# Kernel optimization log

Measured on AMD Instinct MI355X. Metric: run time of the kernel, lower is better.

The kernel has to match this reference:

```python
import jax, jax.numpy as jnp
import numpy as np

RADIUS = 0.4
K = 32
EPS = 1e-5


def ball_query(xyz, new_xyz, radius, k):
    """xyz: (B,N,3), new_xyz: (B,M,3) -> idx (B,M,k) int32.
    Replicates CUDA ball_query: first k points within radius (in index order),
    padded with the first found index."""
    N = xyz.shape[1]
    # squared distances (B,M,N)
    d2 = jnp.sum((new_xyz[:, :, None, :] - xyz[:, None, :, :]) ** 2, axis=-1)
    within = d2 < radius * radius
    order = jnp.arange(N, dtype=jnp.int32)
    key = jnp.where(within, order[None, None, :], N)
    idx_sorted = jnp.argsort(key, axis=-1)[..., :k].astype(jnp.int32)  # (B,M,k)
    cnt = within.sum(axis=-1)  # (B,M)
    first = idx_sorted[..., :1]
    slot = jnp.arange(k)[None, None, :]
    return jnp.where(slot < cnt[..., None], idx_sorted, first)


def gather_bmk(x_bnc, idx):
    """x_bnc: (B,N,C), idx: (B,M,K) -> (B,M,K,C)"""
    return jnp.take_along_axis(x_bnc[:, None, :, :], idx[..., None], axis=2)


def conv_bn_relu(x, w, b, gamma, beta):
    """x: (B,Cin,M,K); w: (Cout,Cin). 1x1 Conv2d + BatchNorm2d (train stats) + ReLU."""
    x = jnp.einsum('bcmk,oc->bomk', x, w) + b[None, :, None, None]
    mu = x.mean(axis=(0, 2, 3), keepdims=True)
    var = x.var(axis=(0, 2, 3), keepdims=True)
    x = gamma[None, :, None, None] * (x - mu) * jax.lax.rsqrt(var + EPS) + beta[None, :, None, None]
    return jax.nn.relu(x)


def setup_inputs() -> dict:
    key = jax.random.key(0)
    ks = jax.random.split(key, 16)
    B, N, C, M = 4, 16384, 128, 1024
    mlp = [131, 128, 128, 256]
    inp = {
        'points_xyz': jax.random.normal(ks[0], (B, N, 3), dtype=jnp.float32),
        'features': jax.random.normal(ks[1], (B, C, N), dtype=jnp.float32),
        'indices': jax.random.randint(ks[2], (B, M), 0, N, dtype=jnp.int32),
    }
    for i in range(3):
        cin, cout = mlp[i], mlp[i + 1]
        inp[f'w{i+1}'] = jax.random.normal(ks[3 + 4 * i], (cout, cin), dtype=jnp.float32) / np.sqrt(cin)
        inp[f'b{i+1}'] = jnp.zeros((cout,), dtype=jnp.float32)
        inp[f'g{i+1}'] = jnp.ones((cout,), dtype=jnp.float32)
        inp[f'beta{i+1}'] = jnp.zeros((cout,), dtype=jnp.float32)
    return inp


def reference(points_xyz, features, indices,
              w1, b1, g1, beta1, w2, b2, g2, beta2, w3, b3, g3, beta3):
    # sample centers: new_xyz (B,M,3)
    new_xyz = jnp.take_along_axis(points_xyz, indices[..., None], axis=1)
    # ball query + group
    idx = ball_query(points_xyz, new_xyz, RADIUS, K)            # (B,M,K)
    grouped_xyz = gather_bmk(points_xyz, idx) - new_xyz[:, :, None, :]  # (B,M,K,3)
    grouped_feat = gather_bmk(features.transpose(0, 2, 1), idx)         # (B,M,K,C)
    x = jnp.concatenate([grouped_xyz, grouped_feat], axis=-1)           # (B,M,K,3+C)
    x = x.transpose(0, 3, 1, 2)                                         # (B,3+C,M,K)
    # shared MLP (1x1 Conv2d + BN + ReLU)
    x = conv_bn_relu(x, w1, b1, g1, beta1)
    x = conv_bn_relu(x, w2, b2, g2, beta2)
    x = conv_bn_relu(x, w3, b3, g3, beta3)
    # max pool over K -> (B, Cout, M)
    new_features = x.max(axis=-1)
    return new_xyz, new_features
```

## Files before the change

kernel.cpp:

```cpp
#include <hip/hip_runtime.h>

#define B_ 4
#define N_ 16384
#define C_ 128
#define M_ 1024
#define K_ 32
#define NTOT (B_*M_*K_)
#define RAD2 0.16f
#define EPS_ 1e-5f

typedef unsigned short ushort_t;
typedef __bf16 bf16x8 __attribute__((ext_vector_type(8)));
typedef float f32x4 __attribute__((ext_vector_type(4)));

__device__ __forceinline__ float b2f(ushort_t u){
  unsigned int x = ((unsigned int)u) << 16;
  return __builtin_bit_cast(float, x);
}
__device__ __forceinline__ ushort_t f2b(float f){
  unsigned int u = __builtin_bit_cast(unsigned int, f);
  unsigned int r = (u + 0x7FFFu + ((u >> 16) & 1u)) >> 16;
  return (ushort_t)r;
}

__global__ __launch_bounds__(256) void ball_query_k(
    const float* __restrict__ xyz, const int* __restrict__ indices,
    float* __restrict__ new_xyz, int* __restrict__ idx)
{
  int t = threadIdx.x;
  int wv = t >> 6, lane = t & 63;
  int g = blockIdx.x*4 + wv;
  int b = g >> 10;
  const float* pb = xyz + (size_t)b*N_*3;
  const float4* pb4 = (const float4*)pb;
  int qi = indices[g];
  float qx = pb[qi*3+0], qy = pb[qi*3+1], qz = pb[qi*3+2];
  if (lane < 3) new_xyz[g*3 + lane] = pb[qi*3 + lane];

  int cnt = 0, firstIdx = 0;
  int* op = idx + g*K_;

  float4 buf0[6], buf1[6];
  #pragma unroll
  for (int i = 0; i < 6; i++) buf0[i] = pb4[lane*6 + i];

  auto process = [&](const float4* buf, int chunk){
    const float* f = (const float*)buf;
    unsigned int local_mask = 0;
    #pragma unroll
    for (int j = 0; j < 8; j++){
      float dx = f[j*3+0]-qx, dy = f[j*3+1]-qy, dz = f[j*3+2]-qz;
      if (dx*dx + dy*dy + dz*dz < RAD2) local_mask |= (1u << j);
    }
    if (__ballot(local_mask != 0) == 0ull) return;
    int base = chunk*512;
    int lcnt = __popc(local_mask);
    int incl = lcnt;
    #pragma unroll
    for (int d = 1; d < 64; d <<= 1){
      int tt = __shfl_up(incl, d);
      if (lane >= d) incl += tt;
    }
    int excl = incl - lcnt;
    int total = __shfl(incl, 63);
    if (cnt == 0){
      int lf = local_mask ? (lane*8 + __builtin_ctz(local_mask)) : 0x7fffffff;
      #pragma unroll
      for (int d = 1; d < 64; d <<= 1) lf = min(lf, __shfl_xor(lf, d));
      firstIdx = base + lf;
    }
    int sl = cnt + excl;
    unsigned int m = local_mask;
    while (m && sl < K_){
      int j = __builtin_ctz(m); m &= m - 1u;
      op[sl++] = base + lane*8 + j;
    }
    cnt += total;
  };

  for (int chunk = 0; chunk < 32; chunk += 2){
    if (chunk + 1 < 32){
      #pragma unroll
      for (int i = 0; i < 6; i++) buf1[i] = pb4[(chunk+1)*384 + lane*6 + i];
    }
    process(buf0, chunk);
    if (cnt >= K_) break;
    if (chunk + 2 < 32){
      #pragma unroll
      for (int i = 0; i < 6; i++) buf0[i] = pb4[(chunk+2)*384 + lane*6 + i];
    }
    process(buf1, chunk + 1);
    if (cnt >= K_) break;
  }
  if (cnt < K_){
    for (int s = cnt + lane; s < K_; s += 64) op[s] = firstIdx;
  }
}

__global__ __launch_bounds__(256) void transpose_feat_k(
    const float* __restrict__ feat, ushort_t* __restrict__ ftr_t)
{
  __shared__ float T[32][133];
  int bi = blockIdx.x;
  int b = bi >> 9, ntile = bi & 511;
  int n0 = ntile * 32;
  int t = threadIdx.x;
  int nl = t & 31;
  #pragma unroll
  for (int ci = 0; ci < 16; ci++){
    int c = ci*8 + (t >> 5);
    T[nl][c] = feat[((size_t)b*C_ + c)*N_ + n0 + nl];
  }
  __syncthreads();
  #pragma unroll
  for (int ii = 0; ii < 2; ii++){
    int v = ii*256 + t;
    int n2 = v >> 4, seg = v & 15;
    union { ushort_t u[8]; uint4 q; } pk;
    #pragma unroll
    for (int j = 0; j < 8; j++) pk.u[j] = f2b(T[n2][seg*8 + j]);
    *(uint4*)(ftr_t + ((size_t)b*N_ + n0 + n2)*C_ + seg*8) = pk.q;
  }
}

__global__ __launch_bounds__(256) void prep_w_k(
    const float* __restrict__ w1, const float* __restrict__ w2, const float* __restrict__ w3,
    ushort_t* __restrict__ W1b, ushort_t* __restrict__ W2b, ushort_t* __restrict__ W3b)
{
  const int T1 = 128*160, T2 = 128*128, T3 = 256*128;
  for (int e = blockIdx.x*256 + threadIdx.x; e < T1+T2+T3; e += gridDim.x*256){
    if (e < T1){
      int o = e / 160, c = e % 160;
      float v = 0.f;
      if (c < 128) v = w1[o*131 + 3 + c];
      else if (c < 131) v = w1[o*131 + (c - 128)];
      W1b[e] = f2b(v);
    } else if (e < T1+T2){
      int e2 = e - T1;
      W2b[e2] = f2b(w2[e2]);
    } else {
      int e3 = e - T1 - T2;
      W3b[e3] = f2b(w3[e3]);
    }
  }
}

__global__ __launch_bounds__(256, 2) void conv1_k(
    const float* __restrict__ xyz, const ushort_t* __restrict__ ftr_t,
    const int* __restrict__ idx, const float* __restrict__ new_xyz,
    const ushort_t* __restrict__ W1b, const float* __restrict__ b1,
    ushort_t* __restrict__ Y1, float* __restrict__ sumO, float* __restrict__ sqO)
{
  __shared__ alignas(16) ushort_t Xs[32*168];
  __shared__ alignas(16) float Ys[32*68];
  int t = threadIdx.x;
  int wv = t >> 6, lane = t & 63, quad = lane >> 4, l15 = lane & 15;
  int row = t >> 3, chunk = t & 7;
  int col0 = (blockIdx.x & 1) * 64;
  int blk = blockIdx.x >> 1;

  if (t < 128){
    int rr = t >> 2, cc = t & 3;
    *(uint4*)(Xs + rr*168 + 128 + cc*8) = make_uint4(0,0,0,0);
  }
  bf16x8 wf[5];
  #pragma unroll
  for (int kt = 0; kt < 5; kt++)
    wf[kt] = *(const bf16x8*)(W1b + (col0 + wv*16 + l15)*160 + kt*32 + quad*8);
  float bs_r = b1[col0 + wv*16 + l15];
  float s = 0.f, s2 = 0.f;

  const int GPB = 8;
  int g0 = blk * GPB;
  int b = g0 >> 10;
  int ia[GPB], ibv[GPB];
  #pragma unroll
  for (int i = 0; i < GPB; i++){
    ia[i]  = idx[(g0+i)*K_ + row];
    ibv[i] = idx[(g0+i)*K_ + (t & 31)];
  }
  for (int i = 0; i < GPB; i++){
    int g = g0 + i;
    const ushort_t* src = ftr_t + ((size_t)b*N_ + ia[i])*C_ + chunk*16;
    uint4 q0 = *(const uint4*)src;
    uint4 q1 = *(const uint4*)(src + 8);
    *(uint4*)(Xs + row*168 + chunk*16) = q0;
    *(uint4*)(Xs + row*168 + chunk*16 + 8) = q1;
    if (t < 32){
      const float* pp = xyz + ((size_t)b*N_ + ibv[i])*3;
      const float* qq = new_xyz + (size_t)g*3;
      unsigned int u0 = (unsigned int)f2b(pp[0]-qq[0]) | ((unsigned int)f2b(pp[1]-qq[1]) << 16);
      unsigned int u1 = (unsigned int)f2b(pp[2]-qq[2]);
      *(uint2*)(Xs + t*168 + 128) = make_uint2(u0, u1);
    }
    __syncthreads();
    bf16x8 af[2][5];
    #pragma unroll
    for (int mt = 0; mt < 2; mt++)
      #pragma unroll
      for (int kt = 0; kt < 5; kt++)
        af[mt][kt] = *(const bf16x8*)(Xs + (mt*16 + l15)*168 + kt*32 + quad*8);
    f32x4 acc[2] = {(f32x4){0,0,0,0}, (f32x4){0,0,0,0}};
    #pragma unroll
    for (int kt = 0; kt < 5; kt++){
      acc[0] = __builtin_amdgcn_mfma_f32_16x16x32_bf16(af[0][kt], wf[kt], acc[0], 0,0,0);
      acc[1] = __builtin_amdgcn_mfma_f32_16x16x32_bf16(af[1][kt], wf[kt], acc[1], 0,0,0);
    }
    {
      int o = wv*16 + l15;
      #pragma unroll
      for (int mt = 0; mt < 2; mt++)
        #pragma unroll
        for (int r = 0; r < 4; r++){
          float v = acc[mt][r] + bs_r;
          s += v; s2 += v*v;
          Ys[(mt*16 + quad*4 + r)*68 + o] = v;
        }
    }
    __syncthreads();
    {
      const float* yp = &Ys[row*68 + chunk*8];
      f32x4 y0 = *(const f32x4*)(yp);
      f32x4 y1 = *(const f32x4*)(yp + 4);
      union { ushort_t u[8]; uint4 q; } p0;
      #pragma unroll
      for (int j = 0; j < 4; j++){
        p0.u[j] = f2b(y0[j]); p0.u[4+j] = f2b(y1[j]);
      }
      *(uint4*)(Y1 + ((size_t)g*K_ + row)*128 + col0 + chunk*8) = p0.q;
    }
  }
  s  += __shfl_xor(s, 16);  s  += __shfl_xor(s, 32);
  s2 += __shfl_xor(s2, 16); s2 += __shfl_xor(s2, 32);
  if (quad == 0){
    int o = col0 + wv*16 + l15;
    atomicAdd(&sumO[o], s);
    atomicAdd(&sqO[o], s2);
  }
}

template<int COUT, bool MAXMIN>
__global__ __launch_bounds__(256, 2) void convB_k(
    const ushort_t* __restrict__ Yin, const ushort_t* __restrict__ Wb,
    const float* __restrict__ bias, const float* __restrict__ g_bn,
    const float* __restrict__ beta_bn, const float* __restrict__ sumI,
    const float* __restrict__ sqI, ushort_t* __restrict__ Yout,
    unsigned int* __restrict__ Ymm, float* __restrict__ sumO, float* __restrict__ sqO)
{
  constexpr int HALF = COUT/2;
  constexpr int NT = HALF/64;
  constexpr int NXS = MAXMIN ? 2 : 1;
  __shared__ alignas(16) ushort_t Xs[NXS][32*136];
  __shared__ alignas(16) float Ys[MAXMIN ? 4 : 32*68];
  int t = threadIdx.x;
  int wv = t >> 6, lane = t & 63, quad = lane >> 4, l15 = lane & 15;
  int row = t >> 3, chunk = t & 7;
  int col0 = (blockIdx.x & 1) * HALF;
  int blk = blockIdx.x >> 1;

  float a_r[16], d_r[16];
  #pragma unroll
  for (int j = 0; j < 16; j++){
    int c = chunk*16 + j;
    float mu  = sumI[c] * (1.f/NTOT);
    float var = sqI[c]  * (1.f/NTOT) - mu*mu;
    float a = g_bn[c] * rsqrtf(var + EPS_);
    a_r[j] = a; d_r[j] = beta_bn[c] - a*mu;
  }
  bf16x8 wf[NT][4];
  #pragma unroll
  for (int nt = 0; nt < NT; nt++)
    #pragma unroll
    for (int kt = 0; kt < 4; kt++)
      wf[nt][kt] = *(const bf16x8*)(Wb + (col0 + wv*(NT*16) + nt*16 + l15)*128 + kt*32 + quad*8);
  float bs_r[NT];
  #pragma unroll
  for (int nt = 0; nt < NT; nt++) bs_r[nt] = bias[col0 + wv*(NT*16) + nt*16 + l15];
  float s[NT], s2[NT];
  #pragma unroll
  for (int nt = 0; nt < NT; nt++){ s[nt] = 0.f; s2[nt] = 0.f; }

  const int GPB = 8;
  int g0 = blk * GPB;
  uint4 r0, r1;
  {
    const ushort_t* src = Yin + ((size_t)g0*K_ + row)*128 + chunk*16;
    r0 = *(const uint4*)src; r1 = *(const uint4*)(src + 8);
  }
  for (int i = 0; i < GPB; i++){
    int g = g0 + i;
    ushort_t* X = Xs[MAXMIN ? (i & (NXS-1)) : 0];
    union { ushort_t u[8]; uint4 q; } i0, i1, o0, o1;
    i0.q = r0; i1.q = r1;
    #pragma unroll
    for (int j = 0; j < 8; j++){
      o0.u[j] = f2b(fmaxf(a_r[j]  *b2f(i0.u[j]) + d_r[j],   0.f));
      o1.u[j] = f2b(fmaxf(a_r[8+j]*b2f(i1.u[j]) + d_r[8+j], 0.f));
    }
    *(uint4*)(X + row*136 + chunk*16) = o0.q;
    *(uint4*)(X + row*136 + chunk*16 + 8) = o1.q;
    if (i + 1 < GPB){
      const ushort_t* src = Yin + ((size_t)(g+1)*K_ + row)*128 + chunk*16;
      r0 = *(const uint4*)src; r1 = *(const uint4*)(src + 8);
    }
    __syncthreads();
    bf16x8 af[2][4];
    #pragma unroll
    for (int mt = 0; mt < 2; mt++)
      #pragma unroll
      for (int kt = 0; kt < 4; kt++)
        af[mt][kt] = *(const bf16x8*)(X + (mt*16 + l15)*136 + kt*32 + quad*8);
    f32x4 acc[NT][2];
    #pragma unroll
    for (int nt = 0; nt < NT; nt++){ acc[nt][0] = (f32x4){0,0,0,0}; acc[nt][1] = (f32x4){0,0,0,0}; }
    #pragma unroll
    for (int nt = 0; nt < NT; nt++)
      #pragma unroll
      for (int kt = 0; kt < 4; kt++){
        acc[nt][0] = __builtin_amdgcn_mfma_f32_16x16x32_bf16(af[0][kt], wf[nt][kt], acc[nt][0], 0,0,0);
        acc[nt][1] = __builtin_amdgcn_mfma_f32_16x16x32_bf16(af[1][kt], wf[nt][kt], acc[nt][1], 0,0,0);
      }
    if constexpr (!MAXMIN){
      {
        int o = wv*16 + l15;
        #pragma unroll
        for (int mt = 0; mt < 2; mt++)
          #pragma unroll
          for (int r = 0; r < 4; r++){
            float v = acc[0][mt][r] + bs_r[0];
            s[0] += v; s2[0] += v*v;
            Ys[(mt*16 + quad*4 + r)*68 + o] = v;
          }
      }
      __syncthreads();
      const float* yp = &Ys[row*68 + chunk*8];
      f32x4 y0 = *(const f32x4*)(yp);
      f32x4 y1 = *(const f32x4*)(yp + 4);
      union { ushort_t u[8]; uint4 q; } p0;
      #pragma unroll
      for (int j = 0; j < 4; j++){
        p0.u[j] = f2b(y0[j]); p0.u[4+j] = f2b(y1[j]);
      }
      *(uint4*)(Yout + ((size_t)g*K_ + row)*128 + col0 + chunk*8) = p0.q;
    } else {
      #pragma unroll
      for (int nt = 0; nt < NT; nt++){
        float v0 = acc[nt][0][0] + bs_r[nt];
        float mx = v0, mn = v0;
        s[nt] += v0; s2[nt] += v0*v0;
        #pragma unroll
        for (int mt = 0; mt < 2; mt++)
          #pragma unroll
          for (int r = 0; r < 4; r++){
            if (mt == 0 && r == 0) continue;
            float v = acc[nt][mt][r] + bs_r[nt];
            s[nt] += v; s2[nt] += v*v;
            mx = fmaxf(mx, v); mn = fminf(mn, v);
          }
        mx = fmaxf(mx, __shfl_xor(mx, 16)); mx = fmaxf(mx, __shfl_xor(mx, 32));
        mn = fminf(mn, __shfl_xor(mn, 16)); mn = fminf(mn, __shfl_xor(mn, 32));
        if (quad == 0){
          int o = col0 + wv*(NT*16) + nt*16 + l15;
          Ymm[(size_t)g*256 + o] = (unsigned int)f2b(mx) | ((unsigned int)f2b(mn) << 16);
        }
      }
    }
  }
  #pragma unroll
  for (int nt = 0; nt < NT; nt++){
    s[nt]  += __shfl_xor(s[nt], 16);  s[nt]  += __shfl_xor(s[nt], 32);
    s2[nt] += __shfl_xor(s2[nt], 16); s2[nt] += __shfl_xor(s2[nt], 32);
    if (quad == 0){
      int o = col0 + wv*(NT*16) + nt*16 + l15;
      atomicAdd(&sumO[o], s[nt]);
      atomicAdd(&sqO[o], s2[nt]);
    }
  }
}

__global__ __launch_bounds__(256) void finalize_k(
    const unsigned int* __restrict__ Ymm, const float* __restrict__ g3,
    const float* __restrict__ beta3, const float* __restrict__ sum3,
    const float* __restrict__ sq3, float* __restrict__ out)
{
  __shared__ float T[16][264];
  __shared__ float abn[256], dbn[256];
  int t = threadIdx.x;
  int b = blockIdx.x >> 6;
  int m0 = (blockIdx.x & 63) * 16;
  {
    float mu  = sum3[t] * (1.f/NTOT);
    float var = sq3[t]  * (1.f/NTOT) - mu*mu;
    float a = g3[t] * rsqrtf(var + EPS_);
    abn[t] = a; dbn[t] = beta3[t] - a*mu;
  }
  __syncthreads();
  #pragma unroll
  for (int i = 0; i < 4; i++){
    int v4 = i*256 + t;
    int m = v4 >> 6, oq = (v4 & 63) * 4;
    uint4 w = *(const uint4*)(Ymm + ((size_t)(b*M_ + m0 + m))*256 + oq);
    unsigned int wsv[4] = {w.x, w.y, w.z, w.w};
    float r[4];
    #pragma unroll
    for (int j = 0; j < 4; j++){
      int o = oq + j;
      float mx = b2f((ushort_t)(wsv[j] & 0xffffu));
      float mn = b2f((ushort_t)(wsv[j] >> 16));
      float a = abn[o];
      float val = (a >= 0.f) ? (a*mx + dbn[o]) : (a*mn + dbn[o]);
      r[j] = fmaxf(val, 0.f);
    }
    *(f32x4*)(&T[m][oq]) = *(f32x4*)r;
  }
  __syncthreads();
  #pragma unroll
  for (int p = 0; p < 4; p++){
    int o = p*64 + (t >> 2), c = t & 3;
    float4 v = make_float4(T[c*4+0][o], T[c*4+1][o], T[c*4+2][o], T[c*4+3][o]);
    *(float4*)(out + ((size_t)(b*256 + o))*M_ + m0 + c*4) = v;
  }
}

extern "C" void kernel_launch(void* const* d_in, const int* in_sizes, int n_in,
                              void* d_out, int out_size, void* d_ws, size_t ws_size,
                              hipStream_t stream)
{
  (void)in_sizes; (void)n_in; (void)out_size; (void)ws_size;
  const float* xyz  = (const float*)d_in[0];
  const float* feat = (const float*)d_in[1];
  const int*   inds = (const int*)d_in[2];
  const float* w1 = (const float*)d_in[3];
  const float* b1 = (const float*)d_in[4];
  const float* g1 = (const float*)d_in[5];
  const float* be1= (const float*)d_in[6];
  const float* w2 = (const float*)d_in[7];
  const float* b2 = (const float*)d_in[8];
  const float* g2 = (const float*)d_in[9];
  const float* be2= (const float*)d_in[10];
  const float* w3 = (const float*)d_in[11];
  const float* b3 = (const float*)d_in[12];
  const float* g3 = (const float*)d_in[13];
  const float* be3= (const float*)d_in[14];

  char* ws = (char*)d_ws;
  float* stats = (float*)ws;
  float* s1sum = stats + 0*256;  float* s1sq = stats + 1*256;
  float* s2sum = stats + 2*256;  float* s2sq = stats + 3*256;
  float* s3sum = stats + 4*256;  float* s3sq = stats + 5*256;
  size_t off = 6*256*sizeof(float);
  int* idx = (int*)(ws + off);                off += (size_t)B_*M_*K_*4;
  ushort_t* ftr_t = (ushort_t*)(ws + off);    off += (size_t)B_*N_*C_*2;
  ushort_t* W1b = (ushort_t*)(ws + off);      off += 128*160*2;
  ushort_t* W2b = (ushort_t*)(ws + off);      off += 128*128*2;
  ushort_t* W3b = (ushort_t*)(ws + off);      off += 256*128*2;
  ushort_t* Y1 = (ushort_t*)(ws + off);       off += (size_t)NTOT*128*2;
  ushort_t* Y2 = (ushort_t*)(ws + off);       off += (size_t)NTOT*128*2;
  unsigned int* Ymm = (unsigned int*)(ws + off); off += (size_t)B_*M_*256*4;

  float* new_xyz  = (float*)d_out;
  float* out_feat = (float*)d_out + (size_t)B_*M_*3;

  hipMemsetAsync(stats, 0, 6*256*sizeof(float), stream);
  prep_w_k<<<272, 256, 0, stream>>>(w1, w2, w3, W1b, W2b, W3b);
  transpose_feat_k<<<2048, 256, 0, stream>>>(feat, ftr_t);
  ball_query_k<<<1024, 256, 0, stream>>>(xyz, inds, new_xyz, idx);
  conv1_k<<<1024, 256, 0, stream>>>(xyz, ftr_t, idx, new_xyz, W1b, b1, Y1, s1sum, s1sq);
  convB_k<128,false><<<1024, 256, 0, stream>>>(Y1, W2b, b2, g1, be1, s1sum, s1sq, Y2, nullptr, s2sum, s2sq);
  convB_k<256,true ><<<1024, 256, 0, stream>>>(Y2, W3b, b3, g2, be2, s2sum, s2sq, nullptr, Ymm, s3sum, s3sq);
  finalize_k<<<256, 256, 0, stream>>>(Ymm, g3, be3, s3sum, s3sq, out_feat);
}
```

Baseline: 220.8 us.

## Merge prep kernels into one launch and double-buffer LDS in conv kernels

Folds weight conversion, feature transpose, ball query and the stats memset into a single block-partitioned kernel, removing three launches and a memset. conv1 now prefetches the next group's gather into registers. conv1 and convB double-buffer the LDS input and output tiles, which drops one __syncthreads per group by deferring each tile's writeback to the next iteration. The bf16 conversion switches to the hardware __bf16 cast. The trade-offs are more LDS per block, which may reduce occupancy, and dependence on the cast rounding the same way as before.

```diff
diff --git a/kernel.cpp b/kernel.cpp
--- a/kernel.cpp
+++ b/kernel.cpp
@@ -18,117 +18,111 @@
   return __builtin_bit_cast(float, x);
 }
 __device__ __forceinline__ ushort_t f2b(float f){
-  unsigned int u = __builtin_bit_cast(unsigned int, f);
-  unsigned int r = (u + 0x7FFFu + ((u >> 16) & 1u)) >> 16;
-  return (ushort_t)r;
-}
-
-__global__ __launch_bounds__(256) void ball_query_k(
+  return __builtin_bit_cast(ushort_t, (__bf16)f);
+}
+
+__global__ __launch_bounds__(256) void prep_all_k(
+    const float* __restrict__ feat, ushort_t* __restrict__ ftr_t,
     const float* __restrict__ xyz, const int* __restrict__ indices,
-    float* __restrict__ new_xyz, int* __restrict__ idx)
-{
-  int t = threadIdx.x;
-  int wv = t >> 6, lane = t & 63;
-  int g = blockIdx.x*4 + wv;
-  int b = g >> 10;
-  const float* pb = xyz + (size_t)b*N_*3;
-  const float4* pb4 = (const float4*)pb;
-  int qi = indices[g];
-  float qx = pb[qi*3+0], qy = pb[qi*3+1], qz = pb[qi*3+2];
-  if (lane < 3) new_xyz[g*3 + lane] = pb[qi*3 + lane];
-
-  int cnt = 0, firstIdx = 0;
-  int* op = idx + g*K_;
-
-  float4 buf0[6], buf1[6];
-  #pragma unroll
-  for (int i = 0; i < 6; i++) buf0[i] = pb4[lane*6 + i];
-
-  auto process = [&](const float4* buf, int chunk){
-    const float* f = (const float*)buf;
-    unsigned int local_mask = 0;
-    #pragma unroll
-    for (int j = 0; j < 8; j++){
-      float dx = f[j*3+0]-qx, dy = f[j*3+1]-qy, dz = f[j*3+2]-qz;
-      if (dx*dx + dy*dy + dz*dz < RAD2) local_mask |= (1u << j);
-    }
-    if (__ballot(local_mask != 0) == 0ull) return;
-    int base = chunk*512;
-    int lcnt = __popc(local_mask);
-    int incl = lcnt;
-    #pragma unroll
-    for (int d = 1; d < 64; d <<= 1){
-      int tt = __shfl_up(incl, d);
-      if (lane >= d) incl += tt;
-    }
-    int excl = incl - lcnt;
-    int total = __shfl(incl, 63);
-    if (cnt == 0){
-      int lf = local_mask ? (lane*8 + __builtin_ctz(local_mask)) : 0x7fffffff;
-      #pragma unroll
-      for (int d = 1; d < 64; d <<= 1) lf = min(lf, __shfl_xor(lf, d));
-      firstIdx = base + lf;
-    }
-    int sl = cnt + excl;
-    unsigned int m = local_mask;
-    while (m && sl < K_){
-      int j = __builtin_ctz(m); m &= m - 1u;
-      op[sl++] = base + lane*8 + j;
-    }
-    cnt += total;
-  };
-
-  for (int chunk = 0; chunk < 32; chunk += 2){
-    if (chunk + 1 < 32){
-      #pragma unroll
-      for (int i = 0; i < 6; i++) buf1[i] = pb4[(chunk+1)*384 + lane*6 + i];
-    }
-    process(buf0, chunk);
-    if (cnt >= K_) break;
-    if (chunk + 2 < 32){
-      #pragma unroll
-      for (int i = 0; i < 6; i++) buf0[i] = pb4[(chunk+2)*384 + lane*6 + i];
-    }
-    process(buf1, chunk + 1);
-    if (cnt >= K_) break;
-  }
-  if (cnt < K_){
-    for (int s = cnt + lane; s < K_; s += 64) op[s] = firstIdx;
-  }
-}
-
-__global__ __launch_bounds__(256) void transpose_feat_k(
-    const float* __restrict__ feat, ushort_t* __restrict__ ftr_t)
+    float* __restrict__ new_xyz, int* __restrict__ idx,
+    const float* __restrict__ w1, const float* __restrict__ w2, const float* __restrict__ w3,
+    ushort_t* __restrict__ W1b, ushort_t* __restrict__ W2b, ushort_t* __restrict__ W3b,
+    float* __restrict__ stats)
 {
   __shared__ float T[32][133];
-  int bi = blockIdx.x;
-  int b = bi >> 9, ntile = bi & 511;
-  int n0 = ntile * 32;
+  int bid = blockIdx.x;
   int t = threadIdx.x;
-  int nl = t & 31;
-  #pragma unroll
-  for (int ci = 0; ci < 16; ci++){
-    int c = ci*8 + (t >> 5);
-    T[nl][c] = feat[((size_t)b*C_ + c)*N_ + n0 + nl];
-  }
-  __syncthreads();
-  #pragma unroll
-  for (int ii = 0; ii < 2; ii++){
-    int v = ii*256 + t;
-    int n2 = v >> 4, seg = v & 15;
-    union { ushort_t u[8]; uint4 q; } pk;
-    #pragma unroll
-    for (int j = 0; j < 8; j++) pk.u[j] = f2b(T[n2][seg*8 + j]);
-    *(uint4*)(ftr_t + ((size_t)b*N_ + n0 + n2)*C_ + seg*8) = pk.q;
-  }
-}
-
-__global__ __launch_bounds__(256) void prep_w_k(
-    const float* __restrict__ w1, const float* __restrict__ w2, const float* __restrict__ w3,
-    ushort_t* __restrict__ W1b, ushort_t* __restrict__ W2b, ushort_t* __restrict__ W3b)
-{
-  const int T1 = 128*160, T2 = 128*128, T3 = 256*128;
-  for (int e = blockIdx.x*256 + threadIdx.x; e < T1+T2+T3; e += gridDim.x*256){
+
+  if (bid < 2048){
+    int b = bid >> 9, ntile = bid & 511;
+    int n0 = ntile * 32;
+    int nl = t & 31;
+    #pragma unroll
+    for (int ci = 0; ci < 16; ci++){
+      int c = ci*8 + (t >> 5);
+      T[nl][c] = feat[((size_t)b*C_ + c)*N_ + n0 + nl];
+    }
+    __syncthreads();
+    #pragma unroll
+    for (int ii = 0; ii < 2; ii++){
+      int v = ii*256 + t;
+      int n2 = v >> 4, seg = v & 15;
+      union { ushort_t u[8]; uint4 q; } pk;
+      #pragma unroll
+      for (int j = 0; j < 8; j++) pk.u[j] = f2b(T[n2][seg*8 + j]);
+      *(uint4*)(ftr_t + ((size_t)b*N_ + n0 + n2)*C_ + seg*8) = pk.q;
+    }
+  } else if (bid < 3072){
+    int wv = t >> 6, lane = t & 63;
+    int g = (bid - 2048)*4 + wv;
+    int b = g >> 10;
+    const float* pb = xyz + (size_t)b*N_*3;
+    const float4* pb4 = (const float4*)pb;
+    int qi = indices[g];
+    float qx = pb[qi*3+0], qy = pb[qi*3+1], qz = pb[qi*3+2];
+    if (lane < 3) new_xyz[g*3 + lane] = pb[qi*3 + lane];
+
+    int cnt = 0, firstIdx = 0;
+    int* op = idx + g*K_;
+
+    float4 buf0[6], buf1[6];
+    #pragma unroll
+    for (int i = 0; i < 6; i++) buf0[i] = pb4[lane*6 + i];
+
+    auto process = [&](const float4* buf, int chunk){
+      const float* f = (const float*)buf;
+      unsigned int local_mask = 0;
+      #pragma unroll
+      for (int j = 0; j < 8; j++){
+        float dx = f[j*3+0]-qx, dy = f[j*3+1]-qy, dz = f[j*3+2]-qz;
+        if (dx*dx + dy*dy + dz*dz < RAD2) local_mask |= (1u << j);
+      }
+      if (__ballot(local_mask != 0) == 0ull) return;
+      int base = chunk*512;
+      int lcnt = __popc(local_mask);
+      int incl = lcnt;
+      #pragma unroll
+      for (int d = 1; d < 64; d <<= 1){
+        int tt = __shfl_up(incl, d);
+        if (lane >= d) incl += tt;
+      }
+      int excl = incl - lcnt;
+      int total = __shfl(incl, 63);
+      if (cnt == 0){
+        int lf = local_mask ? (lane*8 + __builtin_ctz(local_mask)) : 0x7fffffff;
+        #pragma unroll
+        for (int d = 1; d < 64; d <<= 1) lf = min(lf, __shfl_xor(lf, d));
+        firstIdx = base + lf;
+      }
+      int sl = cnt + excl;
+      unsigned int m = local_mask;
+      while (m && sl < K_){
+        int j = __builtin_ctz(m); m &= m - 1u;
+        op[sl++] = base + lane*8 + j;
+      }
+      cnt += total;
+    };
+
+    for (int chunk = 0; chunk < 32; chunk += 2){
+      if (chunk + 1 < 32){
+        #pragma unroll
+        for (int i = 0; i < 6; i++) buf1[i] = pb4[(chunk+1)*384 + lane*6 + i];
+      }
+      process(buf0, chunk);
+      if (cnt >= K_) break;
+      if (chunk + 2 < 32){
+        #pragma unroll
+        for (int i = 0; i < 6; i++) buf0[i] = pb4[(chunk+2)*384 + lane*6 + i];
+      }
+      process(buf1, chunk + 1);
+      if (cnt >= K_) break;
+    }
+    if (cnt < K_){
+      for (int s = cnt + lane; s < K_; s += 64) op[s] = firstIdx;
+    }
+  } else {
+    const int T1 = 128*160, T2 = 128*128;
+    int e = (bid - 3072)*256 + t;
     if (e < T1){
       int o = e / 160, c = e % 160;
       float v = 0.f;
@@ -142,6 +136,10 @@
       int e3 = e - T1 - T2;
       W3b[e3] = f2b(w3[e3]);
     }
+    if (bid == 3072){
+      #pragma unroll
+      for (int j = 0; j < 6; j++) stats[j*256 + t] = 0.f;
+    }
   }
 }
 
@@ -151,8 +149,8 @@
     const ushort_t* __restrict__ W1b, const float* __restrict__ b1,
     ushort_t* __restrict__ Y1, float* __restrict__ sumO, float* __restrict__ sqO)
 {
-  __shared__ alignas(16) ushort_t Xs[32*168];
-  __shared__ alignas(16) float Ys[32*68];
+  __shared__ alignas(16) ushort_t Xs[2][32*168];
+  __shared__ alignas(16) float Ys[2][32*68];
   int t = threadIdx.x;
   int wv = t >> 6, lane = t & 63, quad = lane >> 4, l15 = lane & 15;
   int row = t >> 3, chunk = t & 7;
@@ -161,7 +159,8 @@
 
   if (t < 128){
     int rr = t >> 2, cc = t & 3;
-    *(uint4*)(Xs + rr*168 + 128 + cc*8) = make_uint4(0,0,0,0);
+    *(uint4*)(Xs[0] + rr*168 + 128 + cc*8) = make_uint4(0,0,0,0);
+    *(uint4*)(Xs[1] + rr*168 + 128 + cc*8) = make_uint4(0,0,0,0);
   }
   bf16x8 wf[5];
   #pragma unroll
@@ -179,19 +178,37 @@
     ia[i]  = idx[(g0+i)*K_ + row];
     ibv[i] = idx[(g0+i)*K_ + (t & 31)];
   }
+  uint4 r0, r1;
+  float p3x, p3y, p3z, q3x, q3y, q3z;
+  {
+    const ushort_t* src = ftr_t + ((size_t)b*N_ + ia[0])*C_ + chunk*16;
+    r0 = *(const uint4*)src; r1 = *(const uint4*)(src + 8);
+    if (t < 32){
+      const float* pp = xyz + ((size_t)b*N_ + ibv[0])*3;
+      const float* qq = new_xyz + (size_t)g0*3;
+      p3x = pp[0]; p3y = pp[1]; p3z = pp[2];
+      q3x = qq[0]; q3y = qq[1]; q3z = qq[2];
+    }
+  }
   for (int i = 0; i < GPB; i++){
-    int g = g0 + i;
-    const ushort_t* src = ftr_t + ((size_t)b*N_ + ia[i])*C_ + chunk*16;
-    uint4 q0 = *(const uint4*)src;
-    uint4 q1 = *(const uint4*)(src + 8);
-    *(uint4*)(Xs + row*168 + chunk*16) = q0;
-    *(uint4*)(Xs + row*168 + chunk*16 + 8) = q1;
+    int p = i & 1;
+    ushort_t* X = Xs[p];
+    *(uint4*)(X + row*168 + chunk*16) = r0;
+    *(uint4*)(X + row*168 + chunk*16 + 8) = r1;
     if (t < 32){
-      const float* pp = xyz + ((size_t)b*N_ + ibv[i])*3;
-      const float* qq = new_xyz + (size_t)g*3;
-      unsigned int u0 = (unsigned int)f2b(pp[0]-qq[0]) | ((unsigned int)f2b(pp[1]-qq[1]) << 16);
-      unsigned int u1 = (unsigned int)f2b(pp[2]-qq[2]);
-      *(uint2*)(Xs + t*168 + 128) = make_uint2(u0, u1);
+      unsigned int u0 = (unsigned int)f2b(p3x-q3x) | ((unsigned int)f2b(p3y-q3y) << 16);
+      unsigned int u1 = (unsigned int)f2b(p3z-q3z);
+      *(uint2*)(X + t*168 + 128) = make_uint2(u0, u1);
+    }
+    if (i + 1 < GPB){
+      const ushort_t* src = ftr_t + ((size_t)b*N_ + ia[i+1])*C_ + chunk*16;
+      r0 = *(const uint4*)src; r1 = *(const uint4*)(src + 8);
+      if (t < 32){
+        const float* pp = xyz + ((size_t)b*N_ + ibv[i+1])*3;
+        const float* qq = new_xyz + (size_t)(g0+i+1)*3;
+        p3x = pp[0]; p3y = pp[1]; p3z = pp[2];
+        q3x = qq[0]; q3y = qq[1]; q3z = qq[2];
+      }
     }
     __syncthreads();
     bf16x8 af[2][5];
@@ -199,7 +216,7 @@
     for (int mt = 0; mt < 2; mt++)
       #pragma unroll
       for (int kt = 0; kt < 5; kt++)
-        af[mt][kt] = *(const bf16x8*)(Xs + (mt*16 + l15)*168 + kt*32 + quad*8);
+        af[mt][kt] = *(const bf16x8*)(X + (mt*16 + l15)*168 + kt*32 + quad*8);
     f32x4 acc[2] = {(f32x4){0,0,0,0}, (f32x4){0,0,0,0}};
     #pragma unroll
     for (int kt = 0; kt < 5; kt++){
@@ -208,18 +225,18 @@
     }
     {
       int o = wv*16 + l15;
+      float* Yw = Ys[p];
       #pragma unroll
       for (int mt = 0; mt < 2; mt++)
         #pragma unroll
         for (int r = 0; r < 4; r++){
           float v = acc[mt][r] + bs_r;
           s += v; s2 += v*v;
-          Ys[(mt*16 + quad*4 + r)*68 + o] = v;
+          Yw[(mt*16 + quad*4 + r)*68 + o] = v;
         }
     }
-    __syncthreads();
-    {
-      const float* yp = &Ys[row*68 + chunk*8];
+    if (i > 0){
+      const float* yp = &Ys[p^1][row*68 + chunk*8];
       f32x4 y0 = *(const f32x4*)(yp);
       f32x4 y1 = *(const f32x4*)(yp + 4);
       union { ushort_t u[8]; uint4 q; } p0;
@@ -227,8 +244,20 @@
       for (int j = 0; j < 4; j++){
         p0.u[j] = f2b(y0[j]); p0.u[4+j] = f2b(y1[j]);
       }
-      *(uint4*)(Y1 + ((size_t)g*K_ + row)*128 + col0 + chunk*8) = p0.q;
-    }
+      *(uint4*)(Y1 + ((size_t)(g0+i-1)*K_ + row)*128 + col0 + chunk*8) = p0.q;
+    }
+  }
+  __syncthreads();
+  {
+    const float* yp = &Ys[(GPB-1)&1][row*68 + chunk*8];
+    f32x4 y0 = *(const f32x4*)(yp);
+    f32x4 y1 = *(const f32x4*)(yp + 4);
+    union { ushort_t u[8]; uint4 q; } p0;
+    #pragma unroll
+    for (int j = 0; j < 4; j++){
+      p0.u[j] = f2b(y0[j]); p0.u[4+j] = f2b(y1[j]);
+    }
+    *(uint4*)(Y1 + ((size_t)(g0+GPB-1)*K_ + row)*128 + col0 + chunk*8) = p0.q;
   }
   s  += __shfl_xor(s, 16);  s  += __shfl_xor(s, 32);
   s2 += __shfl_xor(s2, 16); s2 += __shfl_xor(s2, 32);
@@ -249,9 +278,8 @@
 {
   constexpr int HALF = COUT/2;
   constexpr int NT = HALF/64;
-  constexpr int NXS = MAXMIN ? 2 : 1;
-  __shared__ alignas(16) ushort_t Xs[NXS][32*136];
-  __shared__ alignas(16) float Ys[MAXMIN ? 4 : 32*68];
+  __shared__ alignas(16) ushort_t Xs[2][32*136];
+  __shared__ alignas(16) float Ys[MAXMIN ? 1 : 2][MAXMIN ? 4 : 32*68];
   int t = threadIdx.x;
   int wv = t >> 6, lane = t & 63, quad = lane >> 4, l15 = lane & 15;
   int row = t >> 3, chunk = t & 7;
@@ -288,8 +316,9 @@
     r0 = *(const uint4*)src; r1 = *(const uint4*)(src + 8);
   }
   for (int i = 0; i < GPB; i++){
+    int p = i & 1;
     int g = g0 + i;
-    ushort_t* X = Xs[MAXMIN ? (i & (NXS-1)) : 0];
+    ushort_t* X = Xs[p];
     union { ushort_t u[8]; uint4 q; } i0, i1, o0, o1;
     i0.q = r0; i1.q = r1;
     #pragma unroll
@@ -323,25 +352,27 @@
     if constexpr (!MAXMIN){
       {
         int o = wv*16 + l15;
+        float* Yw = Ys[p];
         #pragma unroll
         for (int mt = 0; mt < 2; mt++)
           #pragma unroll
           for (int r = 0; r < 4; r++){
             float v = acc[0][mt][r] + bs_r[0];
             s[0] += v; s2[0] += v*v;
-            Ys[(mt*16 + quad*4 + r)*68 + o] = v;
+            Yw[(mt*16 + quad*4 + r)*68 + o] = v;
           }
       }
-      __syncthreads();
-      const float* yp = &Ys[row*68 + chunk*8];
-      f32x4 y0 = *(const f32x4*)(yp);
-      f32x4 y1 = *(const f32x4*)(yp + 4);
-      union { ushort_t u[8]; uint4 q; } p0;
-      #pragma unroll
-      for (int j = 0; j < 4; j++){
-        p0.u[j] = f2b(y0[j]); p0.u[4+j] = f2b(y1[j]);
-      }
-      *(uint4*)(Yout + ((size_t)g*K_ + row)*128 + col0 + chunk*8) = p0.q;
+      if (i > 0){
+        const float* yp = &Ys[p^1][row*68 + chunk*8];
+        f32x4 y0 = *(const f32x4*)(yp);
+        f32x4 y1 = *(const f32x4*)(yp + 4);
+        union { ushort_t u[8]; uint4 q; } p0;
+        #pragma unroll
+        for (int j = 0; j < 4; j++){
+          p0.u[j] = f2b(y0[j]); p0.u[4+j] = f2b(y1[j]);
+        }
+        *(uint4*)(Yout + ((size_t)(g-1)*K_ + row)*128 + col0 + chunk*8) = p0.q;
+      }
     } else {
       #pragma unroll
       for (int nt = 0; nt < NT; nt++){
@@ -365,6 +396,18 @@
         }
       }
     }
+  }
+  if constexpr (!MAXMIN){
+    __syncthreads();
+    const float* yp = &Ys[(GPB-1)&1][row*68 + chunk*8];
+    f32x4 y0 = *(const f32x4*)(yp);
+    f32x4 y1 = *(const f32x4*)(yp + 4);
+    union { ushort_t u[8]; uint4 q; } p0;
+    #pragma unroll
+    for (int j = 0; j < 4; j++){
+      p0.u[j] = f2b(y0[j]); p0.u[4+j] = f2b(y1[j]);
+    }
+    *(uint4*)(Yout + ((size_t)(g0+GPB-1)*K_ + row)*128 + col0 + chunk*8) = p0.q;
   }
   #pragma unroll
   for (int nt = 0; nt < NT; nt++){
@@ -461,10 +504,8 @@
   float* new_xyz  = (float*)d_out;
   float* out_feat = (float*)d_out + (size_t)B_*M_*3;
 
-  hipMemsetAsync(stats, 0, 6*256*sizeof(float), stream);
-  prep_w_k<<<272, 256, 0, stream>>>(w1, w2, w3, W1b, W2b, W3b);
-  transpose_feat_k<<<2048, 256, 0, stream>>>(feat, ftr_t);
-  ball_query_k<<<1024, 256, 0, stream>>>(xyz, inds, new_xyz, idx);
+  prep_all_k<<<3344, 256, 0, stream>>>(feat, ftr_t, xyz, inds, new_xyz, idx,
+                                       w1, w2, w3, W1b, W2b, W3b, stats);
   conv1_k<<<1024, 256, 0, stream>>>(xyz, ftr_t, idx, new_xyz, W1b, b1, Y1, s1sum, s1sq);
   convB_k<128,false><<<1024, 256, 0, stream>>>(Y1, W2b, b2, g1, be1, s1sum, s1sq, Y2, nullptr, s2sum, s2sq);
   convB_k<256,true ><<<1024, 256, 0, stream>>>(Y2, W3b, b3, g2, be2, s2sum, s2sq, nullptr, Ymm, s3sum, s3sq);
```

After: 217.6 us. About the same (-1.5%).
